# Kernel tuning notes

Measured on AMD Instinct MI355X. Metric: run time of the kernel, lower is better.

The kernel has to match this reference:

```python
import jax, jax.numpy as jnp
import numpy as np

T, B, D = 64, 256, 2000
TN, E, H, A, V = 3000, 256, 256, 128, 128
PS, PE, S = 64, 64, 128
G1N, G1L, G2N, G2L = 1500, 4, 1500, 6


def setup_inputs():
    key = jax.random.key(0)
    ks = jax.random.split(key, 32)
    def nrm(k, shape, s=0.05):
        return jax.random.normal(k, shape, dtype=jnp.float32) * s
    inp = {}
    inp["X"] = jax.random.uniform(ks[0], (T, B, D), dtype=jnp.float32)
    inp["profiles"] = nrm(ks[1], (B, PS), 1.0)
    inp["ini_embd"] = nrm(ks[2], (TN, E), 1.0)
    inp["Wa_w"] = nrm(ks[3], (2 * E, A))
    inp["Wa_b"] = jnp.zeros((A,), jnp.float32)
    inp["Ua_w"] = nrm(ks[4], (A, 1))
    inp["gru_Wih"] = nrm(ks[5], (3 * H, E))
    inp["gru_Whh"] = nrm(ks[6], (3 * H, H))
    inp["gru_bih"] = jnp.zeros((3 * H,), jnp.float32)
    inp["gru_bhh"] = jnp.zeros((3 * H,), jnp.float32)
    inp["tranH_w"] = nrm(ks[7], (H + PE, E))
    inp["tranH_b"] = jnp.zeros((E,), jnp.float32)
    inp["out_w"] = nrm(ks[8], (H + V + PE, D))
    inp["out_b"] = jnp.zeros((D,), jnp.float32)
    inp["erase_w"] = nrm(ks[9], (E, V))
    inp["erase_b"] = jnp.zeros((V,), jnp.float32)
    inp["add_w"] = nrm(ks[10], (E, V))
    inp["add_b"] = jnp.zeros((V,), jnp.float32)
    inp["iniVam"] = nrm(ks[11], (S, V), 1.0)
    inp["emP_w"] = nrm(ks[12], (PS, PE))
    inp["emP_b"] = jnp.zeros((PE,), jnp.float32)
    inp["attnP_w"] = nrm(ks[13], (PE + V, PE))
    inp["attnP_b"] = jnp.zeros((PE,), jnp.float32)
    inp["KMIds"] = jax.random.randint(ks[14], (S,), 0, TN, dtype=jnp.int32)
    inp["leaves1"] = jax.random.randint(ks[15], (G1N, G1L), 0, TN, dtype=jnp.int32)
    inp["anc1"] = jax.random.randint(ks[16], (G1N, G1L), 0, TN, dtype=jnp.int32)
    inp["leaves2"] = jax.random.randint(ks[17], (G2N, G2L), 0, TN, dtype=jnp.int32)
    inp["anc2"] = jax.random.randint(ks[18], (G2N, G2L), 0, TN, dtype=jnp.int32)
    inp["mapInfo"] = jax.random.randint(ks[19], (D,), 0, G1N + G2N, dtype=jnp.int32)
    lens = jnp.sort(jax.random.randint(ks[20], (B,), 1, T + 1, dtype=jnp.int32))[::-1]
    inp["X_lengths"] = lens.at[0].set(T)
    return inp


def _forward(floats, ints):
    (X, profiles, ini_embd, Wa_w, Wa_b, Ua_w, gru_Wih, gru_Whh, gru_bih, gru_bhh,
     tranH_w, tranH_b, out_w, out_b, erase_w, erase_b, add_w, add_b, iniVam,
     emP_w, emP_b, attnP_w, attnP_b) = floats
    KMIds, leaves1, anc1, leaves2, anc2, mapInfo, X_lengths = ints

    # GRAM-style ontology attention over (leaf, ancestor) pairs, grouped by path length
    def group_embed(leaves, anc):
        le = ini_embd[leaves]                                     # [N,L,E]
        ae = ini_embd[anc]                                        # [N,L,E]
        hdn = jnp.tanh(jnp.concatenate([le, ae], axis=2) @ Wa_w + Wa_b)
        w = jax.nn.softmax(hdn @ Ua_w, axis=1)                    # [N,L,1]
        return jnp.sum(w * ae, axis=1)                            # [N,E]

    embedMat = jnp.concatenate([group_embed(leaves1, anc1),
                                group_embed(leaves2, anc2)], axis=0)[mapInfo]  # [D,E]
    Xe = jnp.einsum('tbd,de->tbe', X, embedMat)                   # [T,B,E]

    # packed-sequence GRU: frozen state / zero output beyond each sample's length
    mask = (jnp.arange(T)[:, None] < X_lengths[None, :])[..., None]  # [T,B,1]

    def gru_step(h, tup):
        x_t, m_t = tup
        gx = x_t @ gru_Wih.T + gru_bih
        gh = h @ gru_Whh.T + gru_bhh
        r = jax.nn.sigmoid(gx[:, :H] + gh[:, :H])
        z = jax.nn.sigmoid(gx[:, H:2 * H] + gh[:, H:2 * H])
        n = jnp.tanh(gx[:, 2 * H:] + r * gh[:, 2 * H:])
        h_new = (1.0 - z) * n + z * h
        h = jnp.where(m_t, h_new, h)
        return h, jnp.where(m_t, h, 0.0)

    h0 = jnp.zeros((B, H), jnp.float32)
    _, gru_out = jax.lax.scan(gru_step, h0, (Xe, mask))           # [T,B,H]

    prof = profiles @ emP_w + emP_b                               # [B,PE]
    prof_rep = jnp.broadcast_to(prof[None], (T, B, PE))
    tran = jnp.concatenate([gru_out, prof_rep], axis=2) @ tranH_w + tranH_b  # [T,B,E]
    KM = ini_embd[KMIds]                                          # [S,E]
    slot_w = jax.nn.softmax(jnp.einsum('tbe,se->tbs', tran, KM), axis=2)     # [T,B,S]

    # erase/add gates depend only on Xe -> precompute, then scan VM recurrence
    erase = jax.nn.sigmoid(Xe @ erase_w + erase_b)                # [T,B,V]
    add = jnp.tanh(Xe @ add_w + add_b)                            # [T,B,V]

    def mem_step(VM, tup):
        sw, er, ad = tup                                          # [B,S],[B,V],[B,V]
        read = jnp.einsum('bs,bsv->bv', sw, VM)
        VM = VM * (1.0 - sw[:, :, None] * er[:, None, :]) + sw[:, :, None] * ad[:, None, :]
        return VM, read

    VM0 = jnp.broadcast_to(iniVam[None], (B, S, V))
    _, read = jax.lax.scan(mem_step, VM0, (slot_w, erase, add))   # read: [T,B,V]

    attn = jax.nn.relu(jnp.concatenate([prof_rep, read], axis=2) @ attnP_w + attnP_b)
    prof2 = prof_rep * attn
    final = jnp.concatenate([gru_out, read, prof2], axis=2)       # [T,B,H+V+PE]
    # dropout is identity (eval / drop_rate=0)
    return jax.nn.softmax(final @ out_w + out_b, axis=2)          # [T,B,D]


def reference(X, profiles, ini_embd, Wa_w, Wa_b, Ua_w, gru_Wih, gru_Whh, gru_bih, gru_bhh, tranH_w, tranH_b, out_w, out_b, erase_w, erase_b, add_w, add_b, iniVam, emP_w, emP_b, attnP_w, attnP_b, KMIds, leaves1, anc1, leaves2, anc2, mapInfo, X_lengths):
    floats = (X, profiles, ini_embd, Wa_w, Wa_b, Ua_w, gru_Wih, gru_Whh, gru_bih, gru_bhh,
              tranH_w, tranH_b, out_w, out_b, erase_w, erase_b, add_w, add_b, iniVam,
              emP_w, emP_b, attnP_w, attnP_b)
    ints = (KMIds, leaves1, anc1, leaves2, anc2, mapInfo, X_lengths)
    return _forward(floats, ints)
```

## Files before the change

kernel.cpp:

```cpp
#include <hip/hip_runtime.h>
#include <hip/hip_bf16.h>
#include <cmath>

#define T_  64
#define B_  256
#define D_  2000
#define TN_ 3000
#define E_  256
#define H_  256
#define A_  128
#define V_  128
#define PS_ 64
#define PE_ 64
#define S_  128
#define G1N_ 1500
#define G1L_ 4
#define G2N_ 1500
#define G2L_ 6
#define M_  (T_ * B_)
#define KF_ (H_ + V_ + PE_)
#define NREG 28
#define SK_ 4

typedef __attribute__((ext_vector_type(8))) short short8_t;
typedef __attribute__((ext_vector_type(4))) float floatx4;
typedef _Float16 __attribute__((ext_vector_type(2))) h2_t;
typedef _Float16 __attribute__((ext_vector_type(8))) h8_t;

static __device__ __forceinline__ float sigmoidf_(float x) {
    return 1.0f / (1.0f + __expf(-x));
}

static __device__ __forceinline__ void bsplit_(float v, __hip_bfloat16& hi, __hip_bfloat16& lo) {
    hi = __float2bfloat16(v);
    lo = __float2bfloat16(v - __bfloat162float(hi));
}

static __device__ __forceinline__ float dot2_(unsigned int w, unsigned int h, float acc) {
    union { unsigned int u; h2_t h; } cw, ch;
    cw.u = w; ch.u = h;
#if __has_builtin(__builtin_amdgcn_fdot2)
    return __builtin_amdgcn_fdot2(cw.h, ch.h, acc, false);
#else
    return acc + (float)cw.h[0] * (float)ch.h[0] + (float)cw.h[1] * (float)ch.h[1];
#endif
}

template<int DT>
static __device__ __forceinline__ floatx4 mfma16_(short8_t a, short8_t b, floatx4 c) {
    if constexpr (DT == 0) {
        return __builtin_amdgcn_mfma_f32_16x16x32_bf16(a, b, c, 0, 0, 0);
    } else {
        union { short8_t s; h8_t h; } ua, ub;
        ua.s = a; ub.s = b;
        return __builtin_amdgcn_mfma_f32_16x16x32_f16(ua.h, ub.h, c, 0, 0, 0);
    }
}

template<int EPI, bool ACCUM, int OUTMODE, int NPH, int DT>
__global__ __launch_bounds__(256)
void k_mgemm3(const __hip_bfloat16* __restrict__ Ahi, const __hip_bfloat16* __restrict__ Alo,
              const __hip_bfloat16* __restrict__ Bhi, const __hip_bfloat16* __restrict__ Blo,
              const float* __restrict__ bias, float* __restrict__ Cf,
              __hip_bfloat16* __restrict__ Chi, __hip_bfloat16* __restrict__ Clo,
              int K, int Nreal, int nblk)
{
    __shared__ __align__(16) short As[4096];
    __shared__ __align__(16) short Bs[4096];

    const int tid  = threadIdx.x;
    const int lane = tid & 63;
    const int w    = tid >> 6;
    const int wm   = w >> 1, wn = w & 1;
    const int lr   = lane & 15;
    const int lkc  = lane >> 4;

    const int bx = blockIdx.x;
    const int m0 = (bx / nblk) * 128;
    const int n0 = (bx % nblk) * 128;

    const int fa = 2 * w;
    const size_t aoff0 = (size_t)(m0 + fa * 16 + lr) * K + lkc * 8;
    const size_t aoff1 = aoff0 + (size_t)16 * K;
    const size_t boff0 = (size_t)(n0 + fa * 16 + lr) * K + lkc * 8;
    const size_t boff1 = boff0 + (size_t)16 * K;

    floatx4 acc[4][4];
#pragma unroll
    for (int i = 0; i < 4; ++i)
#pragma unroll
        for (int j = 0; j < 4; ++j) acc[i][j] = floatx4{0.f, 0.f, 0.f, 0.f};

#pragma unroll 1
    for (int ph = 0; ph < NPH; ++ph) {
        const __hip_bfloat16* Ap = (ph == 2) ? Alo : Ahi;
        const __hip_bfloat16* Bp = (ph == 1) ? Blo : Bhi;

        short8_t ra0 = *(const short8_t*)(const void*)(Ap + aoff0);
        short8_t ra1 = *(const short8_t*)(const void*)(Ap + aoff1);
        short8_t rb0 = *(const short8_t*)(const void*)(Bp + boff0);
        short8_t rb1 = *(const short8_t*)(const void*)(Bp + boff1);

        for (int k0 = 0; k0 < K; k0 += 32) {
            __syncthreads();
            *(short8_t*)(void*)&As[(fa    ) * 512 + lane * 8] = ra0;
            *(short8_t*)(void*)&As[(fa + 1) * 512 + lane * 8] = ra1;
            *(short8_t*)(void*)&Bs[(fa    ) * 512 + lane * 8] = rb0;
            *(short8_t*)(void*)&Bs[(fa + 1) * 512 + lane * 8] = rb1;
            __syncthreads();

            if (k0 + 32 < K) {
                int kn = k0 + 32;
                ra0 = *(const short8_t*)(const void*)(Ap + aoff0 + kn);
                ra1 = *(const short8_t*)(const void*)(Ap + aoff1 + kn);
                rb0 = *(const short8_t*)(const void*)(Bp + boff0 + kn);
                rb1 = *(const short8_t*)(const void*)(Bp + boff1 + kn);
            }

            short8_t af[4], bf[4];
#pragma unroll
            for (int i = 0; i < 4; ++i)
                af[i] = *(const short8_t*)(const void*)&As[(wm * 4 + i) * 512 + lane * 8];
#pragma unroll
            for (int j = 0; j < 4; ++j)
                bf[j] = *(const short8_t*)(const void*)&Bs[(wn * 4 + j) * 512 + lane * 8];
#pragma unroll
            for (int i = 0; i < 4; ++i)
#pragma unroll
                for (int j = 0; j < 4; ++j)
                    acc[i][j] = mfma16_<DT>(af[i], bf[j], acc[i][j]);
        }
    }

#pragma unroll
    for (int i = 0; i < 4; ++i) {
        const int row = m0 + wm * 64 + i * 16 + (lane >> 4) * 4;
#pragma unroll
        for (int j = 0; j < 4; ++j) {
            const int col = n0 + wn * 64 + j * 16 + (lane & 15);
            if (col < Nreal) {
                float bv = bias ? bias[col] : 0.0f;
#pragma unroll
                for (int r = 0; r < 4; ++r) {
                    float v = acc[i][j][r] + bv;
                    if (EPI == 1) v = (col < 128) ? sigmoidf_(v) : tanhf(v);
                    if (EPI == 2) {
                        if (col < 128) v = sigmoidf_(v);
                        else if (col < 256) v = tanhf(v);
                    }
                    size_t o = (size_t)(row + r) * Nreal + col;
                    if (OUTMODE == 0) {
                        if (ACCUM) v += Cf[o];
                        Cf[o] = v;
                    } else if (OUTMODE == 1) {
                        __hip_bfloat16 h, l;
                        bsplit_(v, h, l);
                        Chi[o] = h; Clo[o] = l;
                    } else {
                        ((_Float16*)Chi)[o] = (_Float16)v;
                    }
                }
            }
        }
    }
}

__global__ __launch_bounds__(256)
void k_mgemmX(const float* __restrict__ A,
              const _Float16* __restrict__ Bhi, const _Float16* __restrict__ Blo,
              float* __restrict__ P4)
{
    const int KP = 2048, KR = 2000, NN = 256, nblk = 2;
    const int KC = 2048 / SK_;
    __shared__ __align__(16) short Ah[4096];
    __shared__ __align__(16) short Bh[4096];
    __shared__ __align__(16) short Bl[4096];

    const int tid  = threadIdx.x;
    const int lane = tid & 63;
    const int w    = tid >> 6;
    const int wm   = w >> 1, wn = w & 1;
    const int lr   = lane & 15;
    const int lkc  = lane >> 4;

    const int kc = blockIdx.x >> 8;
    const int bx = blockIdx.x & 255;
    const int m0 = (bx / nblk) * 128;
    const int n0 = (bx % nblk) * 128;
    const int KC0 = kc * KC;
    float* dst = P4 + (size_t)kc * (M_ * 256);

    const int fa = 2 * w;
    const float* arow0 = A + (size_t)(m0 + fa * 16 + lr) * KR;
    const float* arow1 = arow0 + (size_t)16 * KR;
    const size_t boff0 = (size_t)(n0 + fa * 16 + lr) * KP + lkc * 8;
    const size_t boff1 = boff0 + (size_t)16 * KP;

    floatx4 acc[4][4];
#pragma unroll
    for (int i = 0; i < 4; ++i)
#pragma unroll
        for (int j = 0; j < 4; ++j) acc[i][j] = floatx4{0.f, 0.f, 0.f, 0.f};

    float a0v[8], a1v[8];
    short8_t bh0, bh1, bl0, bl1;

#define LOADA8(ROW, KB, DST)                                                  \
    if ((KB) + 7 < KR) {                                                      \
        float4 p_ = *(const float4*)((ROW) + (KB));                           \
        float4 q_ = *(const float4*)((ROW) + (KB) + 4);                       \
        DST[0]=p_.x; DST[1]=p_.y; DST[2]=p_.z; DST[3]=p_.w;                   \
        DST[4]=q_.x; DST[5]=q_.y; DST[6]=q_.z; DST[7]=q_.w;                   \
    } else {                                                                  \
        _Pragma("unroll")                                                     \
        for (int ii = 0; ii < 8; ++ii)                                        \
            DST[ii] = ((KB) + ii < KR) ? (ROW)[(KB) + ii] : 0.0f;             \
    }

    {
        const int kb = KC0 + lkc * 8;
        LOADA8(arow0, kb, a0v)
        LOADA8(arow1, kb, a1v)
        bh0 = *(const short8_t*)(const void*)(Bhi + boff0 + KC0);
        bh1 = *(const short8_t*)(const void*)(Bhi + boff1 + KC0);
        bl0 = *(const short8_t*)(const void*)(Blo + boff0 + KC0);
        bl1 = *(const short8_t*)(const void*)(Blo + boff1 + KC0);
    }

    for (int k0 = KC0; k0 < KC0 + KC; k0 += 32) {
        __syncthreads();
        {
            short h8a[8], h8b[8];
#pragma unroll
            for (int i = 0; i < 8; ++i) {
                union { _Float16 h; short s; } ca, cb;
                ca.h = (_Float16)a0v[i];
                cb.h = (_Float16)a1v[i];
                h8a[i] = ca.s; h8b[i] = cb.s;
            }
            *(short8_t*)(void*)&Ah[(fa    ) * 512 + lane * 8] = *(short8_t*)h8a;
            *(short8_t*)(void*)&Ah[(fa + 1) * 512 + lane * 8] = *(short8_t*)h8b;
            *(short8_t*)(void*)&Bh[(fa    ) * 512 + lane * 8] = bh0;
            *(short8_t*)(void*)&Bh[(fa + 1) * 512 + lane * 8] = bh1;
            *(short8_t*)(void*)&Bl[(fa    ) * 512 + lane * 8] = bl0;
            *(short8_t*)(void*)&Bl[(fa + 1) * 512 + lane * 8] = bl1;
        }
        __syncthreads();

        if (k0 + 32 < KC0 + KC) {
            const int kb = k0 + 32 + lkc * 8;
            LOADA8(arow0, kb, a0v)
            LOADA8(arow1, kb, a1v)
            bh0 = *(const short8_t*)(const void*)(Bhi + boff0 + k0 + 32);
            bh1 = *(const short8_t*)(const void*)(Bhi + boff1 + k0 + 32);
            bl0 = *(const short8_t*)(const void*)(Blo + boff0 + k0 + 32);
            bl1 = *(const short8_t*)(const void*)(Blo + boff1 + k0 + 32);
        }

        short8_t af[4], bfh[4], bfl[4];
#pragma unroll
        for (int i = 0; i < 4; ++i) {
            af[i]  = *(const short8_t*)(const void*)&Ah[(wm * 4 + i) * 512 + lane * 8];
            bfh[i] = *(const short8_t*)(const void*)&Bh[(wn * 4 + i) * 512 + lane * 8];
        }
#pragma unroll
        for (int i = 0; i < 4; ++i)
#pragma unroll
            for (int j = 0; j < 4; ++j)
                acc[i][j] = mfma16_<1>(af[i], bfh[j], acc[i][j]);
#pragma unroll
        for (int j = 0; j < 4; ++j)
            bfl[j] = *(const short8_t*)(const void*)&Bl[(wn * 4 + j) * 512 + lane * 8];
#pragma unroll
        for (int i = 0; i < 4; ++i)
#pragma unroll
            for (int j = 0; j < 4; ++j)
                acc[i][j] = mfma16_<1>(af[i], bfl[j], acc[i][j]);
    }
#undef LOADA8

#pragma unroll
    for (int i = 0; i < 4; ++i) {
        const int row = m0 + wm * 64 + i * 16 + (lane >> 4) * 4;
#pragma unroll
        for (int j = 0; j < 4; ++j) {
            const int col = n0 + wn * 64 + j * 16 + (lane & 15);
#pragma unroll
            for (int r = 0; r < 4; ++r)
                dst[(size_t)(row + r) * NN + col] = acc[i][j][r];
        }
    }
}

__global__ void k_reduceX(const float* __restrict__ P4,
                          __hip_bfloat16* __restrict__ hi, __hip_bfloat16* __restrict__ lo)
{
    int idx = blockIdx.x * blockDim.x + threadIdx.x;
    if (idx >= M_ * 256) return;
    const size_t CH = (size_t)M_ * 256;
    float v = P4[idx];
#pragma unroll
    for (int c = 1; c < SK_; ++c) v += P4[idx + c * CH];
    bsplit_(v, hi[idx], lo[idx]);
}

template<int BM, int BN, int BK, int TM, int TN>
__global__ __launch_bounds__(256)
void k_gemm(const float* __restrict__ A, const float* __restrict__ B,
            float* __restrict__ C, int M, int N, int K)
{
    __shared__ float As[BK][BM + 4];
    __shared__ float Bs[BK][BN + 4];
    const int tid = threadIdx.y * blockDim.x + threadIdx.x;
    const int m0 = blockIdx.y * BM;
    const int n0 = blockIdx.x * BN;
    float acc[TM][TN];
#pragma unroll
    for (int i = 0; i < TM; ++i)
#pragma unroll
        for (int j = 0; j < TN; ++j) acc[i][j] = 0.0f;
    for (int k0 = 0; k0 < K; k0 += BK) {
#pragma unroll
        for (int i = tid; i < BM * BK; i += 256) {
            int r = i / BK, c = i % BK;
            int m = m0 + r;
            As[c][r] = (m < M) ? A[(size_t)m * K + k0 + c] : 0.0f;
        }
#pragma unroll
        for (int i = tid; i < BK * BN; i += 256) {
            int r = i / BN, c = i % BN;
            Bs[r][c] = B[(size_t)(k0 + r) * N + n0 + c];
        }
        __syncthreads();
#pragma unroll
        for (int kk = 0; kk < BK; ++kk) {
            float a[TM], b[TN];
#pragma unroll
            for (int i = 0; i < TM; ++i) a[i] = As[kk][threadIdx.y * TM + i];
#pragma unroll
            for (int j = 0; j < TN; ++j) b[j] = Bs[kk][threadIdx.x * TN + j];
#pragma unroll
            for (int i = 0; i < TM; ++i)
#pragma unroll
                for (int j = 0; j < TN; ++j) acc[i][j] += a[i] * b[j];
        }
        __syncthreads();
    }
#pragma unroll
    for (int i = 0; i < TM; ++i) {
        int m = m0 + threadIdx.y * TM + i;
        if (m >= M) continue;
#pragma unroll
        for (int j = 0; j < TN; ++j)
            C[(size_t)m * N + n0 + threadIdx.x * TN + j] = acc[i][j];
    }
}

__global__ void k_pack_w2(const float* __restrict__ Wa_w, float* __restrict__ W2)
{
    int idx = blockIdx.x * blockDim.x + threadIdx.x;
    if (idx >= E_ * 2 * A_) return;
    int e = idx / (2 * A_), j = idx % (2 * A_);
    W2[idx] = (j < A_) ? Wa_w[(size_t)e * A_ + j]
                       : Wa_w[(size_t)(E_ + e) * A_ + (j - A_)];
}

__global__ void k_wg_split(const float* __restrict__ erase_w, const float* __restrict__ add_w,
                           const float* __restrict__ Wih,
                           const float* __restrict__ erase_b, const float* __restrict__ add_b,
                           const float* __restrict__ bih,
                           __hip_bfloat16* __restrict__ WGhi, __hip_bfloat16* __restrict__ WGlo,
                           float* __restrict__ biasG)
{
    int idx = blockIdx.x * blockDim.x + threadIdx.x;
    if (idx < 1024 * 256) {
        int n = idx >> 8, k = idx & 255;
        float v;
        if (n < 128)      v = erase_w[(size_t)k * V_ + n];
        else if (n < 256) v = add_w[(size_t)k * V_ + (n - 128)];
        else              v = Wih[(size_t)(n - 256) * 256 + k];
        bsplit_(v, WGhi[idx], WGlo[idx]);
    }
    if (idx < 1024)
        biasG[idx] = (idx < 128) ? erase_b[idx]
                   : (idx < 256) ? add_b[idx - 128]
                                 : bih[idx - 256];
}

__global__ void k_tranHT_split(const float* __restrict__ tranH_w,
                               __hip_bfloat16* __restrict__ hi, __hip_bfloat16* __restrict__ lo)
{
    int idx = blockIdx.x * blockDim.x + threadIdx.x;
    if (idx >= 256 * 320) return;
    int n = idx / 320, k = idx % 320;
    bsplit_(tranH_w[(size_t)k * 256 + n], hi[idx], lo[idx]);
}

__global__ void k_outWT_f16(const float* __restrict__ out_w, _Float16* __restrict__ dst)
{
    int idx = blockIdx.x * blockDim.x + threadIdx.x;
    if (idx >= 2048 * 448) return;
    int n = idx / 448, k = idx % 448;
    float v = (n < D_) ? out_w[(size_t)k * D_ + n] : 0.0f;
    dst[idx] = (_Float16)v;
}

__global__ void k_km_split(const float* __restrict__ ini_embd, const int* __restrict__ KMIds,
                           __hip_bfloat16* __restrict__ hi, __hip_bfloat16* __restrict__ lo)
{
    int idx = blockIdx.x * blockDim.x + threadIdx.x;
    if (idx >= S_ * E_) return;
    int s = idx / E_, k = idx % E_;
    bsplit_(ini_embd[(size_t)KMIds[s] * E_ + k], hi[idx], lo[idx]);
}

__global__ void k_embMT_f16(const float* __restrict__ embG, const int* __restrict__ mapInfo,
                            _Float16* __restrict__ hi, _Float16* __restrict__ lo)
{
    int idx = blockIdx.x * blockDim.x + threadIdx.x;
    if (idx >= 256 * 2048) return;
    int e = idx >> 11, d = idx & 2047;
    float v = (d < D_) ? embG[(size_t)mapInfo[d] * E_ + e] : 0.0f;
    _Float16 h = (_Float16)v;
    hi[idx] = h;
    lo[idx] = (_Float16)(v - (float)h);
}

__global__ void k_wgru_pack(const float* __restrict__ Whh,
                            unsigned int* __restrict__ Wrg, unsigned int* __restrict__ Wst)
{
    int idx = blockIdx.x * blockDim.x + threadIdx.x;
    if (idx >= 768 * 128) return;
    int j = idx / 128, e2 = idx % 128;
    union { unsigned int u; h2_t h; } c;
    c.h[0] = (_Float16)Whh[(size_t)j * 256 + 2 * e2];
    c.h[1] = (_Float16)Whh[(size_t)j * 256 + 2 * e2 + 1];
    if (e2 < 4 * NREG) {
        Wrg[(size_t)e2 * 768 + j] = c.u;
    } else {
        int ee = e2 - 4 * NREG;
        Wst[((size_t)(ee >> 2) * 768 + j) * 4 + (ee & 3)] = c.u;
    }
}

__global__ void k_prof(const float* __restrict__ profiles, const float* __restrict__ emP_w,
                       const float* __restrict__ emP_b, float* __restrict__ prof)
{
    int b = blockIdx.x, j = threadIdx.x;
    float acc = emP_b[j];
    for (int k = 0; k < PS_; ++k) acc += profiles[(size_t)b * PS_ + k] * emP_w[(size_t)k * PE_ + j];
    prof[(size_t)b * PE_ + j] = acc;
}

__global__ void k_fill_tp(const float* __restrict__ prof,
                          __hip_bfloat16* __restrict__ At_hi, __hip_bfloat16* __restrict__ At_lo)
{
    int idx = blockIdx.x * blockDim.x + threadIdx.x;
    if (idx >= M_ * PE_) return;
    int m = idx >> 6, pe = idx & 63;
    float v = prof[(size_t)(m & (B_ - 1)) * PE_ + pe];
    size_t o = (size_t)m * 320 + 256 + pe;
    bsplit_(v, At_hi[o], At_lo[o]);
}

__global__ void k_group_embed(const float* __restrict__ PP, const float* __restrict__ Wa_b,
                              const float* __restrict__ Ua_w, const float* __restrict__ ini_embd,
                              const int* __restrict__ leaves1, const int* __restrict__ anc1,
                              const int* __restrict__ leaves2, const int* __restrict__ anc2,
                              float* __restrict__ embedG)
{
    int n = blockIdx.x;
    int lane = threadIdx.x;
    const int* lv; const int* ac; int L;
    if (n < G1N_) { L = G1L_; lv = leaves1 + (size_t)n * G1L_; ac = anc1 + (size_t)n * G1L_; }
    else { int n2 = n - G1N_; L = G2L_; lv = leaves2 + (size_t)n2 * G2L_; ac = anc2 + (size_t)n2 * G2L_; }

    float score[6]; int ai[6];
    for (int l = 0; l < L; ++l) {
        int li = lv[l]; int av = ac[l]; ai[l] = av;
        float s = 0.0f;
        for (int a = lane; a < A_; a += 64) {
            float hv = tanhf(PP[(size_t)li * 256 + a] + PP[(size_t)av * 256 + 128 + a] + Wa_b[a]);
            s += hv * Ua_w[a];
        }
        for (int o = 32; o; o >>= 1) s += __shfl_xor(s, o);
        score[l] = s;
    }
    float mx = -1e30f;
    for (int l = 0; l < L; ++l) mx = fmaxf(mx, score[l]);
    float w[6], sum = 0.0f;
    for (int l = 0; l < L; ++l) { w[l] = __expf(score[l] - mx); sum += w[l]; }
    float inv = 1.0f / sum;
    for (int e = lane; e < E_; e += 64) {
        float acc = 0.0f;
        for (int l = 0; l < L; ++l) acc += w[l] * inv * ini_embd[(size_t)ai[l] * E_ + e];
        embedG[(size_t)n * E_ + e] = acc;
    }
}

__global__ __launch_bounds__(768, 3)
void k_gru5(const float* __restrict__ Cg, const unsigned int* __restrict__ Wrg,
            const uint4* __restrict__ Wst, const float* __restrict__ bhh,
            const int* __restrict__ X_len, float* __restrict__ gruo,
            __hip_bfloat16* __restrict__ At_hi, __hip_bfloat16* __restrict__ At_lo)
{
    const int b = blockIdx.x;
    const int tid = threadIdx.x;

    __shared__ uint4 h2S[32];
    __shared__ float ghS[768];
    __shared__ float gxnS[256];

    if (tid < 128) ((unsigned int*)h2S)[tid] = 0u;

    uint4 Wr[NREG];
#pragma unroll
    for (int c = 0; c < NREG; ++c) {
        Wr[c].x = Wrg[(size_t)(4 * c + 0) * 768 + tid];
        Wr[c].y = Wrg[(size_t)(4 * c + 1) * 768 + tid];
        Wr[c].z = Wrg[(size_t)(4 * c + 2) * 768 + tid];
        Wr[c].w = Wrg[(size_t)(4 * c + 3) * 768 + tid];
    }

    float hreg = 0.0f;
    const int len = X_len[b];
    const float bj = bhh[tid];
    __syncthreads();

    for (int t = 0; t < T_; ++t) {
        float gxv = Cg[((size_t)t * B_ + b) * 1024 + 256 + tid];

        float a0 = bj;
#pragma unroll
        for (int c = 0; c < 32; ++c) {
            uint4 w = (c < NREG) ? Wr[c] : Wst[(size_t)(c - NREG) * 768 + tid];
            uint4 h = h2S[c];
            a0 = dot2_(w.x, h.x, a0);
            a0 = dot2_(w.y, h.y, a0);
            a0 = dot2_(w.z, h.z, a0);
            a0 = dot2_(w.w, h.w, a0);
        }

        if (tid < 512) ghS[tid] = a0 + gxv;
        else { ghS[tid] = a0; gxnS[tid - 512] = gxv; }
        __syncthreads();

        if (tid < 256) {
            float r  = sigmoidf_(ghS[tid]);
            float z  = sigmoidf_(ghS[256 + tid]);
            float nn = tanhf(gxnS[tid] + r * ghS[512 + tid]);
            float hnew = (1.0f - z) * nn + z * hreg;
            bool msk = (t < len);
            hreg = msk ? hnew : hreg;
            float ov = msk ? hreg : 0.0f;
            size_t m = (size_t)t * B_ + b;
            gruo[m * H_ + tid] = ov;
            size_t o = m * 320 + tid;
            bsplit_(ov, At_hi[o], At_lo[o]);
            float partner = __shfl_xor(hreg, 1);
            if (!(tid & 1)) {
                union { unsigned int u; h2_t h; } p;
                p.h[0] = (_Float16)hreg;
                p.h[1] = (_Float16)partner;
                ((unsigned int*)h2S)[tid >> 1] = p.u;
            }
        }
        __syncthreads();
    }
}

__global__ __launch_bounds__(256)
void k_mem(const float* __restrict__ slotw, const float* __restrict__ Cg,
           const float* __restrict__ iniVam, float* __restrict__ readv)
{
    const int b = blockIdx.x;
    const int tid = threadIdx.x;
    const int v = tid & (V_ - 1);
    const int sh = tid >> 7;
    const int sbase = sh * 64;

    float VM[64];
#pragma unroll
    for (int i = 0; i < 64; ++i) VM[i] = iniVam[(size_t)(sbase + i) * V_ + v];

    __shared__ float swL[S_];
    __shared__ float eaL[2 * V_];
    __shared__ float part[V_];

    for (int t = 0; t < T_; ++t) {
        size_t m = (size_t)t * B_ + b;
        if (tid < S_) swL[tid] = slotw[m * S_ + tid];
        eaL[tid] = Cg[m * 1024 + tid];
        __syncthreads();

        float er = eaL[v], ad = eaL[V_ + v];
        float p0 = 0.0f, p1 = 0.0f, p2 = 0.0f, p3 = 0.0f;
#pragma unroll
        for (int i = 0; i < 16; ++i) {
            float s0 = swL[sbase + 4 * i];
            float s1 = swL[sbase + 4 * i + 1];
            float s2 = swL[sbase + 4 * i + 2];
            float s3 = swL[sbase + 4 * i + 3];
            float v0 = VM[4 * i], v1 = VM[4 * i + 1], v2 = VM[4 * i + 2], v3 = VM[4 * i + 3];
            p0 += s0 * v0; p1 += s1 * v1; p2 += s2 * v2; p3 += s3 * v3;
            VM[4 * i]     = v0 * (1.0f - s0 * er) + s0 * ad;
            VM[4 * i + 1] = v1 * (1.0f - s1 * er) + s1 * ad;
            VM[4 * i + 2] = v2 * (1.0f - s2 * er) + s2 * ad;
            VM[4 * i + 3] = v3 * (1.0f - s3 * er) + s3 * ad;
        }
        float acc = (p0 + p1) + (p2 + p3);
        if (sh == 1) part[v] = acc;
        __syncthreads();
        if (sh == 0) readv[m * V_ + v] = acc + part[v];
        __syncthreads();
    }
}

__global__ __launch_bounds__(256)
void k_build_final(const float* __restrict__ gruo, const float* __restrict__ readv,
                   const float* __restrict__ prof, const float* __restrict__ attnP_w,
                   const float* __restrict__ attnP_b, _Float16* __restrict__ F)
{
    const int m = blockIdx.x;
    const int b = m & (B_ - 1);
    const int tid = threadIdx.x;
    __shared__ float rd[V_];
    __shared__ float pf[PE_];
    if (tid < V_) rd[tid] = readv[(size_t)m * V_ + tid];
    if (tid < PE_) pf[tid] = prof[(size_t)b * PE_ + tid];
    __syncthreads();

    size_t base = (size_t)m * KF_;
    F[base + tid] = (_Float16)gruo[(size_t)m * H_ + tid];
    if (tid < V_) F[base + H_ + tid] = (_Float16)rd[tid];
    if (tid < PE_) {
        float a = attnP_b[tid];
        for (int k = 0; k < PE_; ++k) a += pf[k] * attnP_w[(size_t)k * PE_ + tid];
        for (int k = 0; k < V_; ++k) a += rd[k] * attnP_w[(size_t)(PE_ + k) * PE_ + tid];
        a = fmaxf(a, 0.0f);
        F[base + H_ + V_ + tid] = (_Float16)(pf[tid] * a);
    }
}

__global__ void k_softmax128(float* __restrict__ C)
{
    const int m = blockIdx.x;
    const size_t base = (size_t)m * S_;
    const int lane = threadIdx.x;
    float a = C[base + lane], b = C[base + 64 + lane];
    float mx = fmaxf(a, b);
    for (int o = 32; o; o >>= 1) mx = fmaxf(mx, __shfl_xor(mx, o));
    float e0 = __expf(a - mx), e1 = __expf(b - mx);
    float s = e0 + e1;
    for (int o = 32; o; o >>= 1) s += __shfl_xor(s, o);
    float inv = 1.0f / s;
    C[base + lane] = e0 * inv;
    C[base + 64 + lane] = e1 * inv;
}

__global__ __launch_bounds__(256)
void k_softmax2000(const _Float16* __restrict__ L, float* __restrict__ C)
{
    const int m = blockIdx.x;
    const size_t base = (size_t)m * D_;
    const int tid = threadIdx.x;
    const int wid = tid >> 6, lane = tid & 63;
    __shared__ float red[4], red2[4];

    float v[8];
#pragma unroll
    for (int i = 0; i < 8; ++i) {
        int d = i * 256 + tid;
        v[i] = (d < D_) ? (float)L[base + d] : -1e30f;
    }
    float mx = v[0];
#pragma unroll
    for (int i = 1; i < 8; ++i) mx = fmaxf(mx, v[i]);
    for (int o = 32; o; o >>= 1) mx = fmaxf(mx, __shfl_xor(mx, o));
    if (lane == 0) red[wid] = mx;
    __syncthreads();
    mx = fmaxf(fmaxf(red[0], red[1]), fmaxf(red[2], red[3]));

    float sum = 0.0f;
#pragma unroll
    for (int i = 0; i < 8; ++i) { v[i] = __expf(v[i] - mx); sum += v[i]; }
    for (int o = 32; o; o >>= 1) sum += __shfl_xor(sum, o);
    if (lane == 0) red2[wid] = sum;
    __syncthreads();
    sum = red2[0] + red2[1] + red2[2] + red2[3];
    float inv = 1.0f / sum;
#pragma unroll
    for (int i = 0; i < 8; ++i) {
        int d = i * 256 + tid;
        if (d < D_) C[base + d] = v[i] * inv;
    }
}

extern "C" void kernel_launch(void* const* d_in, const int* in_sizes, int n_in,
                              void* d_out, int out_size, void* d_ws, size_t ws_size,
                              hipStream_t stream)
{
    const float* X        = (const float*)d_in[0];
    const float* profiles = (const float*)d_in[1];
    const float* ini_embd = (const float*)d_in[2];
    const float* Wa_w     = (const float*)d_in[3];
    const float* Wa_b     = (const float*)d_in[4];
    const float* Ua_w     = (const float*)d_in[5];
    const float* gru_Wih  = (const float*)d_in[6];
    const float* gru_Whh  = (const float*)d_in[7];
    const float* gru_bih  = (const float*)d_in[8];
    const float* gru_bhh  = (const float*)d_in[9];
    const float* tranH_w  = (const float*)d_in[10];
    const float* tranH_b  = (const float*)d_in[11];
    const float* out_w    = (const float*)d_in[12];
    const float* out_b    = (const float*)d_in[13];
    const float* erase_w  = (const float*)d_in[14];
    const float* erase_b  = (const float*)d_in[15];
    const float* add_w    = (const float*)d_in[16];
    const float* add_b    = (const float*)d_in[17];
    const float* iniVam   = (const float*)d_in[18];
    const float* emP_w    = (const float*)d_in[19];
    const float* emP_b    = (const float*)d_in[20];
    const float* attnP_w  = (const float*)d_in[21];
    const float* attnP_b  = (const float*)d_in[22];
    const int* KMIds   = (const int*)d_in[23];
    const int* leaves1 = (const int*)d_in[24];
    const int* anc1    = (const int*)d_in[25];
    const int* leaves2 = (const int*)d_in[26];
    const int* anc2    = (const int*)d_in[27];
    const int* mapInfo = (const int*)d_in[28];
    const int* X_len   = (const int*)d_in[29];

    char* ws = (char*)d_ws;
    float* out = (float*)d_out;
    typedef __hip_bfloat16 bf16;

    const size_t R0 = 0;
    const size_t R1 = 67108864;
    const size_t R2 = 83886080;
    const size_t R3 = 100663296;
    size_t P = 121634816;
    const size_t EMBHI = P; P += 1048576;
    const size_t EMBLO = P; P += 1048576;
    const size_t OWF  = P; P += 1835008;
    const size_t WGHI = P; P += 524288;
    const size_t WGLO = P; P += 524288;
    const size_t THHI = P; P += 163840;
    const size_t THLO = P; P += 163840;
    const size_t KMHI = P; P += 65536;
    const size_t KMLO = P; P += 65536;
    const size_t WRG  = P; P += 344064;
    const size_t WST  = P; P += 49152;
    const size_t PROF = P; P += 65536;
    const size_t BIAS = P; P += 4096;
    const size_t W2O  = P; P += 262144;

    float* PP      = (float*)(ws + R0);
    float* embG    = (float*)(ws + R0 + 12288000);
    float* P4      = (float*)(ws + R0);
    float* Cg      = (float*)(ws + R0);
    _Float16* F16  = (_Float16*)(ws + R0);
    _Float16* LG16 = (_Float16*)(ws + 16777216);
    float* gruo    = (float*)(ws + R1);
    bf16*  Xe_hi   = (bf16*)(ws + R2);
    bf16*  Xe_lo   = (bf16*)(ws + R2 + 8388608);
    bf16*  tran_hi = (bf16*)(ws + R2);
    bf16*  tran_lo = (bf16*)(ws + R2 + 8388608);
    bf16*  At_hi   = (bf16*)(ws + R3);
    bf16*  At_lo   = (bf16*)(ws + R3 + 10485760);
    float* slotw   = (float*)(ws + R3);
    float* readv   = (float*)(ws + R3 + 10485760);
    _Float16* EMBhi = (_Float16*)(ws + EMBHI);
    _Float16* EMBlo = (_Float16*)(ws + EMBLO);
    _Float16* OWf = (_Float16*)(ws + OWF);
    bf16*  WGhi = (bf16*)(ws + WGHI); bf16* WGlo = (bf16*)(ws + WGLO);
    bf16*  THhi = (bf16*)(ws + THHI); bf16* THlo = (bf16*)(ws + THLO);
    bf16*  KMhi = (bf16*)(ws + KMHI); bf16* KMlo = (bf16*)(ws + KMLO);
    unsigned int* Wrg = (unsigned int*)(ws + WRG);
    unsigned int* Wst = (unsigned int*)(ws + WST);
    float* prof  = (float*)(ws + PROF);
    float* biasG = (float*)(ws + BIAS);
    float* W2p   = (float*)(ws + W2O);

    k_pack_w2<<<(E_ * 2 * A_ + 255) / 256, 256, 0, stream>>>(Wa_w, W2p);
    k_wg_split<<<(1024 * 256 + 255) / 256, 256, 0, stream>>>(
        erase_w, add_w, gru_Wih, erase_b, add_b, gru_bih, WGhi, WGlo, biasG);
    k_tranHT_split<<<(256 * 320 + 255) / 256, 256, 0, stream>>>(tranH_w, THhi, THlo);
    k_outWT_f16<<<(2048 * 448 + 255) / 256, 256, 0, stream>>>(out_w, OWf);
    k_km_split<<<(S_ * E_ + 255) / 256, 256, 0, stream>>>(ini_embd, KMIds, KMhi, KMlo);
    k_wgru_pack<<<(768 * 128 + 255) / 256, 256, 0, stream>>>(gru_Whh, Wrg, Wst);
    k_prof<<<B_, PE_, 0, stream>>>(profiles, emP_w, emP_b, prof);

    {
        dim3 blk(16, 16);
        dim3 grid(4, (TN_ + 63) / 64);
        k_gemm<64, 64, 16, 4, 4><<<grid, blk, 0, stream>>>(ini_embd, W2p, PP, TN_, 256, E_);
    }
    k_group_embed<<<G1N_ + G2N_, 64, 0, stream>>>(PP, Wa_b, Ua_w, ini_embd,
                                                  leaves1, anc1, leaves2, anc2, embG);
    k_embMT_f16<<<(256 * 2048) / 256, 256, 0, stream>>>(embG, mapInfo, EMBhi, EMBlo);

    k_mgemmX<<<SK_ * 256, 256, 0, stream>>>(X, EMBhi, EMBlo, P4);
    k_reduceX<<<(M_ * 256) / 256, 256, 0, stream>>>(P4, Xe_hi, Xe_lo);

    k_mgemm3<2, false, 0, 3, 0><<<128 * 8, 256, 0, stream>>>(Xe_hi, Xe_lo, WGhi, WGlo,
        biasG, Cg, nullptr, nullptr, 256, 1024, 8);

    k_gru5<<<256, 768, 0, stream>>>(Cg, Wrg, (const uint4*)Wst, gru_bhh, X_len,
                                    gruo, At_hi, At_lo);
    k_fill_tp<<<(M_ * PE_) / 256, 256, 0, stream>>>(prof, At_hi, At_lo);

    k_mgemm3<0, false, 1, 3, 0><<<128 * 2, 256, 0, stream>>>(At_hi, At_lo, THhi, THlo,
        tranH_b, nullptr, tran_hi, tran_lo, 320, 256, 2);

    k_mgemm3<0, false, 0, 3, 0><<<128 * 1, 256, 0, stream>>>(tran_hi, tran_lo, KMhi, KMlo,
        nullptr, slotw, nullptr, nullptr, 256, 128, 1);

    k_softmax128<<<M_, 64, 0, stream>>>(slotw);
    k_mem<<<B_, 256, 0, stream>>>(slotw, Cg, iniVam, readv);
    k_build_final<<<M_, 256, 0, stream>>>(gruo, readv, prof, attnP_w, attnP_b, F16);

    k_mgemm3<0, false, 2, 1, 1><<<128 * 16, 256, 0, stream>>>(
        (const bf16*)F16, nullptr, (const bf16*)OWf, nullptr,
        out_b, nullptr, (bf16*)LG16, nullptr, 448, 2000, 16);

    k_softmax2000<<<M_, 256, 0, stream>>>(LG16, out);
}
```

Measured before the change: 654.6 us.

## Pre-convert X to fp16, drop split-K, use direct global-to-LDS loads

A new pass converts X to padded fp16 once. The X-embedding GEMM then reads fp16 directly instead of converting fp32 inside the loop, and it drops split-K along with its separate reduction kernel by writing the bf16 hi/lo split in its own epilogue. Both GEMMs now fill LDS with global_load_lds and no longer prefetch into registers. This removes the large partial-sum buffer and the reduce pass, but it gives up register double-buffering and cuts the X GEMM grid to 256 blocks, which may lower occupancy.

```diff
diff --git a/kernel.cpp b/kernel.cpp
--- a/kernel.cpp
+++ b/kernel.cpp
@@ -20,7 +20,6 @@
 #define M_  (T_ * B_)
 #define KF_ (H_ + V_ + PE_)
 #define NREG 28
-#define SK_ 4
 
 typedef __attribute__((ext_vector_type(8))) short short8_t;
 typedef __attribute__((ext_vector_type(4))) float floatx4;
@@ -46,6 +45,17 @@
 #endif
 }
 
+static __device__ __forceinline__ void gl_lds16(const void* g, void* l)
+{
+#if __has_builtin(__builtin_amdgcn_global_load_lds)
+    __builtin_amdgcn_global_load_lds(
+        (const __attribute__((address_space(1))) void*)g,
+        (__attribute__((address_space(3))) void*)l, 16, 0, 0);
+#else
+    *(short8_t*)l = *(const short8_t*)g;
+#endif
+}
+
 template<int DT>
 static __device__ __forceinline__ floatx4 mfma16_(short8_t a, short8_t b, floatx4 c) {
     if constexpr (DT == 0) {
@@ -96,26 +106,14 @@
         const __hip_bfloat16* Ap = (ph == 2) ? Alo : Ahi;
         const __hip_bfloat16* Bp = (ph == 1) ? Blo : Bhi;
 
-        short8_t ra0 = *(const short8_t*)(const void*)(Ap + aoff0);
-        short8_t ra1 = *(const short8_t*)(const void*)(Ap + aoff1);
-        short8_t rb0 = *(const short8_t*)(const void*)(Bp + boff0);
-        short8_t rb1 = *(const short8_t*)(const void*)(Bp + boff1);
-
+#pragma unroll 1
         for (int k0 = 0; k0 < K; k0 += 32) {
             __syncthreads();
-            *(short8_t*)(void*)&As[(fa    ) * 512 + lane * 8] = ra0;
-            *(short8_t*)(void*)&As[(fa + 1) * 512 + lane * 8] = ra1;
-            *(short8_t*)(void*)&Bs[(fa    ) * 512 + lane * 8] = rb0;
-            *(short8_t*)(void*)&Bs[(fa + 1) * 512 + lane * 8] = rb1;
+            gl_lds16(Ap + aoff0 + k0, &As[(fa    ) * 512 + lane * 8]);
+            gl_lds16(Ap + aoff1 + k0, &As[(fa + 1) * 512 + lane * 8]);
+            gl_lds16(Bp + boff0 + k0, &Bs[(fa    ) * 512 + lane * 8]);
+            gl_lds16(Bp + boff1 + k0, &Bs[(fa + 1) * 512 + lane * 8]);
             __syncthreads();
-
-            if (k0 + 32 < K) {
-                int kn = k0 + 32;
-                ra0 = *(const short8_t*)(const void*)(Ap + aoff0 + kn);
-                ra1 = *(const short8_t*)(const void*)(Ap + aoff1 + kn);
-                rb0 = *(const short8_t*)(const void*)(Bp + boff0 + kn);
-                rb1 = *(const short8_t*)(const void*)(Bp + boff1 + kn);
-            }
 
             short8_t af[4], bf[4];
 #pragma unroll
@@ -166,12 +164,31 @@
 }
 
 __global__ __launch_bounds__(256)
-void k_mgemmX(const float* __restrict__ A,
-              const _Float16* __restrict__ Bhi, const _Float16* __restrict__ Blo,
-              float* __restrict__ P4)
-{
-    const int KP = 2048, KR = 2000, NN = 256, nblk = 2;
-    const int KC = 2048 / SK_;
+void k_cvtX(const float* __restrict__ X, _Float16* __restrict__ XH)
+{
+    int idx = blockIdx.x * blockDim.x + threadIdx.x;
+    if (idx >= M_ * 256) return;
+    int m = idx >> 8, d0 = (idx & 255) * 8;
+    _Float16 h[8];
+    if (d0 + 7 < D_) {
+        float4 p = *(const float4*)(X + (size_t)m * D_ + d0);
+        float4 q = *(const float4*)(X + (size_t)m * D_ + d0 + 4);
+        h[0]=(_Float16)p.x; h[1]=(_Float16)p.y; h[2]=(_Float16)p.z; h[3]=(_Float16)p.w;
+        h[4]=(_Float16)q.x; h[5]=(_Float16)q.y; h[6]=(_Float16)q.z; h[7]=(_Float16)q.w;
+    } else {
+#pragma unroll
+        for (int i = 0; i < 8; ++i)
+            h[i] = (d0 + i < D_) ? (_Float16)X[(size_t)m * D_ + d0 + i] : (_Float16)0.0f;
+    }
+    *(short8_t*)(XH + (size_t)m * 2048 + d0) = *(short8_t*)h;
+}
+
+__global__ __launch_bounds__(256)
+void k_mgemmXh(const _Float16* __restrict__ XH,
+               const _Float16* __restrict__ Bhi, const _Float16* __restrict__ Blo,
+               __hip_bfloat16* __restrict__ Chi, __hip_bfloat16* __restrict__ Clo)
+{
+    const int KP = 2048, NN = 256, nblk = 2;
     __shared__ __align__(16) short Ah[4096];
     __shared__ __align__(16) short Bh[4096];
     __shared__ __align__(16) short Bl[4096];
@@ -183,16 +200,13 @@
     const int lr   = lane & 15;
     const int lkc  = lane >> 4;
 
-    const int kc = blockIdx.x >> 8;
-    const int bx = blockIdx.x & 255;
+    const int bx = blockIdx.x;
     const int m0 = (bx / nblk) * 128;
     const int n0 = (bx % nblk) * 128;
-    const int KC0 = kc * KC;
-    float* dst = P4 + (size_t)kc * (M_ * 256);
 
     const int fa = 2 * w;
-    const float* arow0 = A + (size_t)(m0 + fa * 16 + lr) * KR;
-    const float* arow1 = arow0 + (size_t)16 * KR;
+    const size_t aoff0 = (size_t)(m0 + fa * 16 + lr) * KP + lkc * 8;
+    const size_t aoff1 = aoff0 + (size_t)16 * KP;
     const size_t boff0 = (size_t)(n0 + fa * 16 + lr) * KP + lkc * 8;
     const size_t boff1 = boff0 + (size_t)16 * KP;
 
@@ -202,60 +216,16 @@
 #pragma unroll
         for (int j = 0; j < 4; ++j) acc[i][j] = floatx4{0.f, 0.f, 0.f, 0.f};
 
-    float a0v[8], a1v[8];
-    short8_t bh0, bh1, bl0, bl1;
-
-#define LOADA8(ROW, KB, DST)                                                  \
-    if ((KB) + 7 < KR) {                                                      \
-        float4 p_ = *(const float4*)((ROW) + (KB));                           \
-        float4 q_ = *(const float4*)((ROW) + (KB) + 4);                       \
-        DST[0]=p_.x; DST[1]=p_.y; DST[2]=p_.z; DST[3]=p_.w;                   \
-        DST[4]=q_.x; DST[5]=q_.y; DST[6]=q_.z; DST[7]=q_.w;                   \
-    } else {                                                                  \
-        _Pragma("unroll")                                                     \
-        for (int ii = 0; ii < 8; ++ii)                                        \
-            DST[ii] = ((KB) + ii < KR) ? (ROW)[(KB) + ii] : 0.0f;             \
-    }
-
-    {
-        const int kb = KC0 + lkc * 8;
-        LOADA8(arow0, kb, a0v)
-        LOADA8(arow1, kb, a1v)
-        bh0 = *(const short8_t*)(const void*)(Bhi + boff0 + KC0);
-        bh1 = *(const short8_t*)(const void*)(Bhi + boff1 + KC0);
-        bl0 = *(const short8_t*)(const void*)(Blo + boff0 + KC0);
-        bl1 = *(const short8_t*)(const void*)(Blo + boff1 + KC0);
-    }
-
-    for (int k0 = KC0; k0 < KC0 + KC; k0 += 32) {
-        __syncthreads();
-        {
-            short h8a[8], h8b[8];
-#pragma unroll
-            for (int i = 0; i < 8; ++i) {
-                union { _Float16 h; short s; } ca, cb;
-                ca.h = (_Float16)a0v[i];
-                cb.h = (_Float16)a1v[i];
-                h8a[i] = ca.s; h8b[i] = cb.s;
-            }
-            *(short8_t*)(void*)&Ah[(fa    ) * 512 + lane * 8] = *(short8_t*)h8a;
-            *(short8_t*)(void*)&Ah[(fa + 1) * 512 + lane * 8] = *(short8_t*)h8b;
-            *(short8_t*)(void*)&Bh[(fa    ) * 512 + lane * 8] = bh0;
-            *(short8_t*)(void*)&Bh[(fa + 1) * 512 + lane * 8] = bh1;
-            *(short8_t*)(void*)&Bl[(fa    ) * 512 + lane * 8] = bl0;
-            *(short8_t*)(void*)&Bl[(fa + 1) * 512 + lane * 8] = bl1;
-        }
-        __syncthreads();
-
-        if (k0 + 32 < KC0 + KC) {
-            const int kb = k0 + 32 + lkc * 8;
-            LOADA8(arow0, kb, a0v)
-            LOADA8(arow1, kb, a1v)
-            bh0 = *(const short8_t*)(const void*)(Bhi + boff0 + k0 + 32);
-            bh1 = *(const short8_t*)(const void*)(Bhi + boff1 + k0 + 32);
-            bl0 = *(const short8_t*)(const void*)(Blo + boff0 + k0 + 32);
-            bl1 = *(const short8_t*)(const void*)(Blo + boff1 + k0 + 32);
-        }
+#pragma unroll 1
+    for (int k0 = 0; k0 < KP; k0 += 32) {
+        __syncthreads();
+        gl_lds16(XH  + aoff0 + k0, &Ah[(fa    ) * 512 + lane * 8]);
+        gl_lds16(XH  + aoff1 + k0, &Ah[(fa + 1) * 512 + lane * 8]);
+        gl_lds16(Bhi + boff0 + k0, &Bh[(fa    ) * 512 + lane * 8]);
+        gl_lds16(Bhi + boff1 + k0, &Bh[(fa + 1) * 512 + lane * 8]);
+        gl_lds16(Blo + boff0 + k0, &Bl[(fa    ) * 512 + lane * 8]);
+        gl_lds16(Blo + boff1 + k0, &Bl[(fa + 1) * 512 + lane * 8]);
+        __syncthreads();
 
         short8_t af[4], bfh[4], bfl[4];
 #pragma unroll
@@ -277,7 +247,6 @@
             for (int j = 0; j < 4; ++j)
                 acc[i][j] = mfma16_<1>(af[i], bfl[j], acc[i][j]);
     }
-#undef LOADA8
 
 #pragma unroll
     for (int i = 0; i < 4; ++i) {
@@ -286,22 +255,15 @@
         for (int j = 0; j < 4; ++j) {
             const int col = n0 + wn * 64 + j * 16 + (lane & 15);
 #pragma unroll
-            for (int r = 0; r < 4; ++r)
-                dst[(size_t)(row + r) * NN + col] = acc[i][j][r];
-        }
-    }
-}
-
-__global__ void k_reduceX(const float* __restrict__ P4,
-                          __hip_bfloat16* __restrict__ hi, __hip_bfloat16* __restrict__ lo)
-{
-    int idx = blockIdx.x * blockDim.x + threadIdx.x;
-    if (idx >= M_ * 256) return;
-    const size_t CH = (size_t)M_ * 256;
-    float v = P4[idx];
-#pragma unroll
-    for (int c = 1; c < SK_; ++c) v += P4[idx + c * CH];
-    bsplit_(v, hi[idx], lo[idx]);
+            for (int r = 0; r < 4; ++r) {
+                float v = acc[i][j][r];
+                size_t o = (size_t)(row + r) * NN + col;
+                __hip_bfloat16 h, l;
+                bsplit_(v, h, l);
+                Chi[o] = h; Clo[o] = l;
+            }
+        }
+    }
 }
 
 template<int BM, int BN, int BK, int TM, int TN>
@@ -757,7 +719,7 @@
 
     float* PP      = (float*)(ws + R0);
     float* embG    = (float*)(ws + R0 + 12288000);
-    float* P4      = (float*)(ws + R0);
+    _Float16* XH   = (_Float16*)(ws + R0);
     float* Cg      = (float*)(ws + R0);
     _Float16* F16  = (_Float16*)(ws + R0);
     _Float16* LG16 = (_Float16*)(ws + 16777216);
@@ -800,8 +762,9 @@
                                                   leaves1, anc1, leaves2, anc2, embG);
     k_embMT_f16<<<(256 * 2048) / 256, 256, 0, stream>>>(embG, mapInfo, EMBhi, EMBlo);
 
-    k_mgemmX<<<SK_ * 256, 256, 0, stream>>>(X, EMBhi, EMBlo, P4);
-    k_reduceX<<<(M_ * 256) / 256, 256, 0, stream>>>(P4, Xe_hi, Xe_lo);
+    k_cvtX<<<(M_ * 256) / 256, 256, 0, stream>>>(X, XH);
+
+    k_mgemmXh<<<128 * 2, 256, 0, stream>>>(XH, EMBhi, EMBlo, Xe_hi, Xe_lo);
 
     k_mgemm3<2, false, 0, 3, 0><<<128 * 8, 256, 0, stream>>>(Xe_hi, Xe_lo, WGhi, WGlo,
         biasG, Cg, nullptr, nullptr, 256, 1024, 8);
```

Result: slower. 691.5 us (+5.6%).
